# Performance work log

Hardware: AMD Instinct MI355X
Metric: run time of the kernel (lower is better)

The kernel has to match this reference:

```python
import jax, jax.numpy as jnp
import numpy as np

B, C, L, P, S = 8, 128, 4096, 16, 8
PC = (L - P) // S + 1  # 511 patches


def setup_inputs() -> dict:
    key = jax.random.key(0)
    k0, k1, k2, k3, k4 = jax.random.split(key, 5)
    x = jax.random.normal(k0, (B, C, L), jnp.float32)
    # offset MLP: Conv1d(1,64,P) == [64,P] matmul; Conv1d(64,2,1) == [2,64] matmul
    w1 = jax.random.normal(k1, (64, P), jnp.float32) * 0.02
    b1 = jax.random.normal(k2, (64,), jnp.float32) * 0.02
    w2 = jax.random.normal(k3, (2, 64), jnp.float32) * 0.02
    b2 = jax.random.normal(k4, (2,), jnp.float32) * 0.02
    return {"x": x, "w1": w1, "b1": b1, "w2": w2, "b2": b2}


def reference(x, w1, b1, w2, b2):
    Bb, Cc, Ll = x.shape
    # --- OffsetPredictor: unfold into [B,C,PC,P] patches, tiny per-patch MLP ---
    idx = jnp.arange(PC)[:, None] * S + jnp.arange(P)[None, :]        # [PC,P]
    patches = x[:, :, idx]                                            # [B,C,PC,P]
    h = jnp.einsum('bcpi,oi->bcpo', patches, w1) + b1                 # [B,C,PC,64]
    h = jax.nn.gelu(h, approximate=False)                             # torch GELU = exact erf
    rel = jnp.einsum('bcpo,ko->bcpk', h, w2) + b2                     # [B,C,PC,2]
    # --- BoxCoder.decode ---
    size_bias = (P - 1) / 2
    anchor = jnp.arange(PC, dtype=jnp.float32) * S + 0.5 * (P - 1)    # [PC]
    dx = rel[..., 0]
    ds = jax.nn.relu(rel[..., 1] + size_bias)
    lo = jnp.clip((dx + anchor - ds) / (Ll - 1), 0.0, 1.0)            # [B,C,PC]
    hi = jnp.clip((dx + anchor + ds) / (Ll - 1), 0.0, 1.0)
    # --- BoxCoder.meshgrid: linear interpolate (align_corners=True) lo->hi over P points ---
    t = jnp.arange(P, dtype=jnp.float32) / (P - 1)                    # [P]
    xs = lo[..., None] + (hi - lo)[..., None] * t                     # [B,C,PC,P]
    ys = jnp.arange(Cc, dtype=jnp.float32) / (Cc - 1)                 # [C], interp of [0,1]
    # --- grid_sample(image=[B,1,C,L], bilinear, align_corners=True, zeros padding) ---
    gx = (xs - 0.5) * 2.0
    gy = (ys - 0.5) * 2.0
    px = (gx + 1.0) * 0.5 * (Ll - 1)                                  # [B,C,PC,P]
    py = (gy + 1.0) * 0.5 * (Cc - 1)                                  # [C]
    py = jnp.broadcast_to(py[None, :, None, None], px.shape)
    x0 = jnp.floor(px); y0 = jnp.floor(py)
    wx = px - x0; wy = py - y0
    x0i = x0.astype(jnp.int32); y0i = y0.astype(jnp.int32)
    bidx = jnp.arange(Bb)[:, None, None, None]

    def gather(yy, xx):
        valid = (yy >= 0) & (yy < Cc) & (xx >= 0) & (xx < Ll)
        yc = jnp.clip(yy, 0, Cc - 1)
        xc = jnp.clip(xx, 0, Ll - 1)
        return jnp.where(valid, x[bidx, yc, xc], 0.0)

    v00 = gather(y0i, x0i)
    v01 = gather(y0i, x0i + 1)
    v10 = gather(y0i + 1, x0i)
    v11 = gather(y0i + 1, x0i + 1)
    out = ((1 - wy) * (1 - wx) * v00 + (1 - wy) * wx * v01
           + wy * (1 - wx) * v10 + wy * wx * v11)
    return out  # [B, C, PC, P] == torch output after permute(0,2,1,3)
```

## Files before the change

kernel.cpp:

```cpp
#include <hip/hip_runtime.h>
#include <math.h>

#define Bn  8
#define Cn  128
#define Ln  4096
#define Pn  16
#define Sn  8
#define PCn 511

typedef short s16x8 __attribute__((ext_vector_type(8)));
typedef float f32x16 __attribute__((ext_vector_type(16)));

__device__ __forceinline__ int sw(int i) { return i ^ ((i >> 5) & 31); }

__device__ __forceinline__ short f2bf(float f) {
    unsigned u = __builtin_bit_cast(unsigned, f);
    u += 0x7FFFu + ((u >> 16) & 1u);
    return (short)(u >> 16);
}

__device__ __forceinline__ float gelu_poly(float u) {
    float z  = 0.70710678118654752f * u;
    float z2 = z * z;
    float p  = fmaf(z2, fmaf(z2, fmaf(z2, -0.02686617064f, 0.11283791671f),
                             -0.37612638903f), 1.12837916709f);
    float er = z * p;
    float h  = 0.5f * u;
    return fmaf(h, er, h);
}

__global__ __launch_bounds__(512, 4) void depatch_kernel(
    const float* __restrict__ x,
    const float* __restrict__ w1,
    const float* __restrict__ b1,
    const float* __restrict__ w2,
    const float* __restrict__ b2,
    float* __restrict__ out)
{
    __shared__ float  ldsA[Ln];
    __shared__ float  ldsB[Ln];
    __shared__ float4 coef[64];

    const int bc   = blockIdx.x;
    const int c    = bc & (Cn - 1);
    const int b    = bc >> 7;
    const int t    = threadIdx.x;
    const int lane = t & 63;
    const int wv   = t >> 6;
    const int half = lane >> 5;
    const int lc   = lane & 31;

    float ysv = (float)c / 127.0f;
    float gyv = (ysv - 0.5f) * 2.0f;
    float py  = (gyv + 1.0f) * 0.5f * 127.0f;
    float y0f = floorf(py);
    float wy  = py - y0f;
    int   y0  = (int)y0f;
    int   y1  = y0 + 1;
    bool  rowBvalid = (y1 < Cn);

    const float* rowA = x + ((size_t)b * Cn + y0) * Ln;
    const float* rowB = x + ((size_t)b * Cn + (rowBvalid ? y1 : (Cn - 1))) * Ln;

    #pragma unroll
    for (int q = 0; q < 4; q++) {
        int id   = q * 512 + t;
        bool isA = (id < 1024);
        int col4 = id & 1023;
        const float* src = isA ? rowA : rowB;
        float4 v = reinterpret_cast<const float4*>(src)[col4];
        if (!isA && !rowBvalid) { v.x = 0.f; v.y = 0.f; v.z = 0.f; v.w = 0.f; }
        float* dst = isA ? ldsA : ldsB;
        int e = col4 * 4;
        dst[sw(e + 0)] = v.x;
        dst[sw(e + 1)] = v.y;
        dst[sw(e + 2)] = v.z;
        dst[sw(e + 3)] = v.w;
    }
    if (t < 64) coef[t] = make_float4(b1[t], w2[t], w2[64 + t], 0.f);

    s16x8 afrag[2];
    #pragma unroll
    for (int h = 0; h < 2; h++) {
        const float* wp = w1 + (32 * h + lc) * 16 + 8 * half;
        float4 qa = reinterpret_cast<const float4*>(wp)[0];
        float4 qb = reinterpret_cast<const float4*>(wp)[1];
        afrag[h][0] = f2bf(qa.x); afrag[h][1] = f2bf(qa.y);
        afrag[h][2] = f2bf(qa.z); afrag[h][3] = f2bf(qa.w);
        afrag[h][4] = f2bf(qb.x); afrag[h][5] = f2bf(qb.y);
        afrag[h][6] = f2bf(qb.z); afrag[h][7] = f2bf(qb.w);
    }
    __syncthreads();

    const float* rowC = (y0 == c) ? ldsA : ldsB;
    s16x8 bfrag[2];
    #pragma unroll
    for (int n = 0; n < 2; n++) {
        int p = 64 * wv + 32 * n + lc;
        if (p > 510) p = 510;
        int e0 = 8 * p + 8 * half;
        #pragma unroll
        for (int j = 0; j < 8; j++)
            bfrag[n][j] = f2bf(rowC[sw(e0 + j)]);
    }

    float rel[2][2] = {{0.f, 0.f}, {0.f, 0.f}};
    #pragma unroll
    for (int h = 0; h < 2; h++) {
        f32x16 z = {};
        f32x16 d0 = __builtin_amdgcn_mfma_f32_32x32x16_bf16(afrag[h], bfrag[0], z, 0, 0, 0);
        f32x16 d1 = __builtin_amdgcn_mfma_f32_32x32x16_bf16(afrag[h], bfrag[1], z, 0, 0, 0);
        #pragma unroll
        for (int r = 0; r < 16; r++) {
            int hid = (r & 3) + 8 * (r >> 2) + 4 * half + 32 * h;
            float4 cf = coef[hid];
            float g0 = gelu_poly(d0[r] + cf.x);
            float g1 = gelu_poly(d1[r] + cf.x);
            rel[0][0] = fmaf(cf.y, g0, rel[0][0]);
            rel[0][1] = fmaf(cf.z, g0, rel[0][1]);
            rel[1][0] = fmaf(cf.y, g1, rel[1][0]);
            rel[1][1] = fmaf(cf.z, g1, rel[1][1]);
        }
    }
    #pragma unroll
    for (int n = 0; n < 2; n++) {
        #pragma unroll
        for (int k = 0; k < 2; k++)
            rel[n][k] += __shfl_xor(rel[n][k], 32, 64);
    }
    float rel0 = (half ? rel[1][0] : rel[0][0]) + b2[0];
    float rel1 = (half ? rel[1][1] : rel[0][1]) + b2[1];

    if (t < PCn) {
        const int p = t;

        float anchor = (float)p * 8.0f + 7.5f;
        float dx = rel0;
        float ds = fmaxf(rel1 + 7.5f, 0.0f);
        float lo = ((dx + anchor) - ds) / 4095.0f;
        float hi = ((dx + anchor) + ds) / 4095.0f;
        lo = fminf(fmaxf(lo, 0.0f), 1.0f);
        hi = fminf(fmaxf(hi, 0.0f), 1.0f);
        float dlh = hi - lo;
        float omwy = 1.0f - wy;

        float* op = out + ((size_t)bc * PCn + p) * Pn;
        #pragma unroll
        for (int q = 0; q < 4; q++) {
            float r[4];
            #pragma unroll
            for (int k = 0; k < 4; k++) {
                int   i   = q * 4 + k;
                float t01 = (float)i / 15.0f;
                float xs = lo + dlh * t01;
                float gx = (xs - 0.5f) * 2.0f;
                float px = (gx + 1.0f) * 0.5f * 4095.0f;
                float x0f = floorf(px);
                float wx  = px - x0f;
                int   x0  = (int)x0f;
                int   x1  = x0 + 1;

                int sx0 = sw(x0);
                float v00 = ldsA[sx0];
                float v10 = ldsB[sx0];
                float v01 = 0.f, v11 = 0.f;
                if (x1 < Ln) {
                    int sx1 = sw(x1);
                    v01 = ldsA[sx1];
                    v11 = ldsB[sx1];
                }

                r[k] = omwy * (1.0f - wx) * v00
                     + omwy * wx          * v01
                     + wy   * (1.0f - wx) * v10
                     + wy   * wx          * v11;
            }
            float4 v; v.x = r[0]; v.y = r[1]; v.z = r[2]; v.w = r[3];
            reinterpret_cast<float4*>(op)[q] = v;
        }
    }
}

extern "C" void kernel_launch(void* const* d_in, const int* in_sizes, int n_in,
                              void* d_out, int out_size, void* d_ws, size_t ws_size,
                              hipStream_t stream) {
    const float* x  = (const float*)d_in[0];
    const float* w1 = (const float*)d_in[1];
    const float* b1 = (const float*)d_in[2];
    const float* w2 = (const float*)d_in[3];
    const float* b2 = (const float*)d_in[4];
    float* out = (float*)d_out;

    dim3 grid(Bn * Cn);
    depatch_kernel<<<grid, 512, 0, stream>>>(x, w1, b1, w2, b2, out);
}
```

Baseline: 95.30 us.

## Drop the redundant second sampled row and pack the GELU polynomial into 2-wide FMAs

The vertical grid_sample coordinate maps channel c onto row c itself, so the y weight is essentially zero. The kernel now loads only its own row into LDS and does 1-D linear interpolation, which halves LDS footprint, row loads and gather reads. The GELU/erf polynomial is rewritten with different coefficients and evaluated on pairs of values using packed fma on 2-wide float vectors. Risks: slight numeric differences if float rounding of the y coordinate is not exactly integral, and a changed GELU approximation.

```diff
diff --git a/kernel.cpp b/kernel.cpp
--- a/kernel.cpp
+++ b/kernel.cpp
@@ -10,6 +10,7 @@
 
 typedef short s16x8 __attribute__((ext_vector_type(8)));
 typedef float f32x16 __attribute__((ext_vector_type(16)));
+typedef float f32x2  __attribute__((ext_vector_type(2)));
 
 __device__ __forceinline__ int sw(int i) { return i ^ ((i >> 5) & 31); }
 
@@ -19,15 +20,16 @@
     return (short)(u >> 16);
 }
 
-__device__ __forceinline__ float gelu_poly(float u) {
-    float z  = 0.70710678118654752f * u;
-    float z2 = z * z;
-    float p  = fmaf(z2, fmaf(z2, fmaf(z2, -0.02686617064f, 0.11283791671f),
-                             -0.37612638903f), 1.12837916709f);
-    float er = z * p;
-    float h  = 0.5f * u;
-    return fmaf(h, er, h);
+#if __has_builtin(__builtin_elementwise_fma)
+__device__ __forceinline__ f32x2 pk_fma(f32x2 a, f32x2 b, f32x2 c) {
+    return __builtin_elementwise_fma(a, b, c);
 }
+#else
+__device__ __forceinline__ f32x2 pk_fma(f32x2 a, f32x2 b, f32x2 c) {
+    f32x2 r; r.x = fmaf(a.x, b.x, c.x); r.y = fmaf(a.y, b.y, c.y); return r;
+}
+#endif
+__device__ __forceinline__ f32x2 pk2(float v) { f32x2 r; r.x = v; r.y = v; return r; }
 
 __global__ __launch_bounds__(512, 4) void depatch_kernel(
     const float* __restrict__ x,
@@ -37,45 +39,27 @@
     const float* __restrict__ b2,
     float* __restrict__ out)
 {
-    __shared__ float  ldsA[Ln];
-    __shared__ float  ldsB[Ln];
+    __shared__ float  ldsC[Ln];
     __shared__ float4 coef[64];
 
     const int bc   = blockIdx.x;
-    const int c    = bc & (Cn - 1);
-    const int b    = bc >> 7;
     const int t    = threadIdx.x;
     const int lane = t & 63;
     const int wv   = t >> 6;
     const int half = lane >> 5;
     const int lc   = lane & 31;
 
-    float ysv = (float)c / 127.0f;
-    float gyv = (ysv - 0.5f) * 2.0f;
-    float py  = (gyv + 1.0f) * 0.5f * 127.0f;
-    float y0f = floorf(py);
-    float wy  = py - y0f;
-    int   y0  = (int)y0f;
-    int   y1  = y0 + 1;
-    bool  rowBvalid = (y1 < Cn);
-
-    const float* rowA = x + ((size_t)b * Cn + y0) * Ln;
-    const float* rowB = x + ((size_t)b * Cn + (rowBvalid ? y1 : (Cn - 1))) * Ln;
+    const float* rowC = x + (size_t)bc * Ln;
 
     #pragma unroll
-    for (int q = 0; q < 4; q++) {
-        int id   = q * 512 + t;
-        bool isA = (id < 1024);
-        int col4 = id & 1023;
-        const float* src = isA ? rowA : rowB;
-        float4 v = reinterpret_cast<const float4*>(src)[col4];
-        if (!isA && !rowBvalid) { v.x = 0.f; v.y = 0.f; v.z = 0.f; v.w = 0.f; }
-        float* dst = isA ? ldsA : ldsB;
+    for (int q = 0; q < 2; q++) {
+        int col4 = q * 512 + t;
+        float4 v = reinterpret_cast<const float4*>(rowC)[col4];
         int e = col4 * 4;
-        dst[sw(e + 0)] = v.x;
-        dst[sw(e + 1)] = v.y;
-        dst[sw(e + 2)] = v.z;
-        dst[sw(e + 3)] = v.w;
+        ldsC[sw(e + 0)] = v.x;
+        ldsC[sw(e + 1)] = v.y;
+        ldsC[sw(e + 2)] = v.z;
+        ldsC[sw(e + 3)] = v.w;
     }
     if (t < 64) coef[t] = make_float4(b1[t], w2[t], w2[64 + t], 0.f);
 
@@ -92,7 +76,6 @@
     }
     __syncthreads();
 
-    const float* rowC = (y0 == c) ? ldsA : ldsB;
     s16x8 bfrag[2];
     #pragma unroll
     for (int n = 0; n < 2; n++) {
@@ -101,10 +84,14 @@
         int e0 = 8 * p + 8 * half;
         #pragma unroll
         for (int j = 0; j < 8; j++)
-            bfrag[n][j] = f2bf(rowC[sw(e0 + j)]);
+            bfrag[n][j] = f2bf(ldsC[sw(e0 + j)]);
     }
 
-    float rel[2][2] = {{0.f, 0.f}, {0.f, 0.f}};
+    const f32x2 q0 = pk2(0.3989422804f), q1 = pk2(-0.0664903801f);
+    const f32x2 q2 = pk2(0.0099735570f), q3 = pk2(-0.0011873282f);
+    const f32x2 hf = pk2(0.5f);
+    f32x2 relA = pk2(0.f);
+    f32x2 relB = pk2(0.f);
     #pragma unroll
     for (int h = 0; h < 2; h++) {
         f32x16 z = {};
@@ -114,22 +101,21 @@
         for (int r = 0; r < 16; r++) {
             int hid = (r & 3) + 8 * (r >> 2) + 4 * half + 32 * h;
             float4 cf = coef[hid];
-            float g0 = gelu_poly(d0[r] + cf.x);
-            float g1 = gelu_poly(d1[r] + cf.x);
-            rel[0][0] = fmaf(cf.y, g0, rel[0][0]);
-            rel[0][1] = fmaf(cf.z, g0, rel[0][1]);
-            rel[1][0] = fmaf(cf.y, g1, rel[1][0]);
-            rel[1][1] = fmaf(cf.z, g1, rel[1][1]);
+            f32x2 u; u.x = d0[r]; u.y = d1[r];
+            u = pk_fma(pk2(1.f), pk2(cf.x), u);
+            f32x2 y  = pk_fma(u, u, pk2(0.f));
+            f32x2 Q  = pk_fma(y, pk_fma(y, pk_fma(y, q3, q2), q1), q0);
+            f32x2 g  = pk_fma(hf, u, pk_fma(y, Q, pk2(0.f)));
+            relA = pk_fma(pk2(cf.y), g, relA);
+            relB = pk_fma(pk2(cf.z), g, relB);
         }
     }
-    #pragma unroll
-    for (int n = 0; n < 2; n++) {
-        #pragma unroll
-        for (int k = 0; k < 2; k++)
-            rel[n][k] += __shfl_xor(rel[n][k], 32, 64);
-    }
-    float rel0 = (half ? rel[1][0] : rel[0][0]) + b2[0];
-    float rel1 = (half ? rel[1][1] : rel[0][1]) + b2[1];
+    relA.x += __shfl_xor(relA.x, 32, 64);
+    relA.y += __shfl_xor(relA.y, 32, 64);
+    relB.x += __shfl_xor(relB.x, 32, 64);
+    relB.y += __shfl_xor(relB.y, 32, 64);
+    float rel0 = (half ? relA.y : relA.x) + b2[0];
+    float rel1 = (half ? relB.y : relB.x) + b2[1];
 
     if (t < PCn) {
         const int p = t;
@@ -142,7 +128,6 @@
         lo = fminf(fmaxf(lo, 0.0f), 1.0f);
         hi = fminf(fmaxf(hi, 0.0f), 1.0f);
         float dlh = hi - lo;
-        float omwy = 1.0f - wy;
 
         float* op = out + ((size_t)bc * PCn + p) * Pn;
         #pragma unroll
@@ -160,20 +145,12 @@
                 int   x0  = (int)x0f;
                 int   x1  = x0 + 1;
 
-                int sx0 = sw(x0);
-                float v00 = ldsA[sx0];
-                float v10 = ldsB[sx0];
-                float v01 = 0.f, v11 = 0.f;
-                if (x1 < Ln) {
-                    int sx1 = sw(x1);
-                    v01 = ldsA[sx1];
-                    v11 = ldsB[sx1];
-                }
+                float v00 = ldsC[sw(x0)];
+                int   xc  = (x1 < Ln) ? x1 : 4095;
+                float v01 = ldsC[sw(xc)];
+                if (x1 >= Ln) v01 = 0.f;
 
-                r[k] = omwy * (1.0f - wx) * v00
-                     + omwy * wx          * v01
-                     + wy   * (1.0f - wx) * v10
-                     + wy   * wx          * v11;
+                r[k] = (1.0f - wx) * v00 + wx * v01;
             }
             float4 v; v.x = r[0]; v.y = r[1]; v.z = r[2]; v.w = r[3];
             reinterpret_cast<float4*>(op)[q] = v;
```

After: 91.14 us. -4.4%, faster.
